# Kernel optimization log

Hardware: AMD Instinct MI355X
Metric: run time of the kernel (lower is better)

Reference implementation:

```python
import jax, jax.numpy as jnp
import numpy as np

# Module hyperparameters (from init_kwargs)
THRESHOLD_BASE = 1.0
TAU_MEM, TAU_SYN, TAU_ADAPT = 0.02, 0.005, 0.1
ADAPT_STRENGTH, HOMEO_RATE, DT = 0.1, 0.01, 0.001


def setup_inputs() -> dict:
    key = jax.random.key(0)
    B, F, T = 32, 8192, 128
    input_current = jax.random.normal(key, (B, F, T), dtype=jnp.float32)
    threshold_scale = jnp.ones((1,), dtype=jnp.float32)   # nn.Parameter(torch.ones(1))
    adaptation_bias = jnp.zeros((1,), dtype=jnp.float32)  # nn.Parameter(torch.zeros(1))
    return {"input_current": input_current,
            "threshold_scale": threshold_scale,
            "adaptation_bias": adaptation_bias}


def reference(input_current, threshold_scale, adaptation_bias):
    """Adaptive-threshold LIF neuron recurrence (AdaptiveThresholdLIFNeuron.forward).

    input_current: [B, F, T]
    Returns (spikes [B,F,T], membrane_trace [T], threshold_trace [T],
             final_firing_rate (scalar EMA), adaptation_state (scalar mean)).
    """
    B, F, T = input_current.shape
    dt = jnp.float32(DT)
    alpha = jnp.exp(-dt / TAU_MEM)   # membrane decay
    beta = jnp.exp(-dt / TAU_SYN)    # synaptic decay
    gamma = jnp.exp(-dt / TAU_ADAPT) # adaptation decay

    I_t = jnp.moveaxis(input_current, -1, 0)  # [T, B, F] for scan over time

    def step(carry, inp):
        membrane, synaptic, adaptation, ema = carry
        synaptic = beta * synaptic + inp
        membrane = alpha * membrane + synaptic
        # homeostatic component uses the running firing-rate EMA (scalar buffer)
        homeo = ADAPT_STRENGTH * jnp.maximum(ema - HOMEO_RATE, 0.0)
        adaptation = gamma * adaptation + (1.0 - gamma) * jax.lax.stop_gradient(membrane)
        threshold = (THRESHOLD_BASE * threshold_scale + homeo
                     + adaptation_bias + 0.1 * adaptation)  # [B, F]
        spike = (membrane >= threshold).astype(membrane.dtype)
        ema = 0.99 * ema + 0.01 * spike.mean()
        membrane = membrane - threshold * spike  # soft reset
        return (membrane, synaptic, adaptation, ema), (spike, membrane.mean(), threshold.mean())

    z = jnp.zeros((B, F), dtype=input_current.dtype)
    init = (z, z, z, jnp.zeros((), dtype=input_current.dtype))
    (membrane, synaptic, adaptation, ema), (spikes_t, mem_trace, thr_trace) = jax.lax.scan(step, init, I_t)

    spikes = jnp.moveaxis(spikes_t, 0, -1)  # [B, F, T]
    return spikes, mem_trace, thr_trace, ema, adaptation.mean()
```

## Files before the change

kernel.cpp:

```cpp
#include <hip/hip_runtime.h>
#include <math.h>

#pragma clang fp contract(off)

typedef unsigned int u32;

#define N_NEUR 262144
#define TT     128
#define OB     ((size_t)N_NEUR * TT)
#define PB     128
#define PT     512
#define NW     8
#define NREP   16
#define WGUARD (1 << 17)

__device__ __forceinline__ float wredf(float v) {
#pragma unroll
  for (int o = 32; o; o >>= 1) v += __shfl_xor(v, o);
  return v;
}
__device__ __forceinline__ int wredi(int v) {
#pragma unroll
  for (int o = 32; o; o >>= 1) v += __shfl_xor(v, o);
  return v;
}

__launch_bounds__(PT)
__global__ void snn_persist(const float* __restrict__ in, const float* __restrict__ tsp,
                            const float* __restrict__ abp, float* __restrict__ out,
                            u32* __restrict__ bits2, u32* __restrict__ g_rep,
                            float* __restrict__ wm, float* __restrict__ wt,
                            float* __restrict__ wa)
{
#pragma clang fp contract(off)
  const int tid  = threadIdx.x;
  const int bid  = blockIdx.x;
  const int gtid = bid * PT + tid;
  const int lane = tid & 63;
  const int wv   = tid >> 6;
  const int rep  = bid & (NREP - 1);

  const float alp = __uint_as_float(0x3F7383C5u);
  const float bet = __uint_as_float(0x3F519856u);
  const float gma = __uint_as_float(0x3F7D73E8u);
  const float omg = 1.0f - gma;
  const float tsv = tsp[0];
  const float abv = abp[0];

  const int n0 = gtid * 4;
  const float4* q0 = (const float4*)(in + (size_t)(n0 + 0) * TT);
  const float4* q1 = (const float4*)(in + (size_t)(n0 + 1) * TT);
  const float4* q2 = (const float4*)(in + (size_t)(n0 + 2) * TT);
  const float4* q3 = (const float4*)(in + (size_t)(n0 + 3) * TT);

  float4 c0 = q0[0], c1 = q1[0], c2 = q2[0], c3 = q3[0];
  float4 f0 = q0[1], f1 = q1[1], f2 = q2[1], f3 = q3[1];

  float S0,S1,S2,S3, Mp0,Mp1,Mp2,Mp3, A0,A1,A2,A3;
  S0 = __builtin_fmaf(bet, 0.0f, c0.x); Mp0 = __builtin_fmaf(alp, 0.0f, S0);
  A0 = __builtin_fmaf(gma, 0.0f, omg * Mp0);
  S1 = __builtin_fmaf(bet, 0.0f, c1.x); Mp1 = __builtin_fmaf(alp, 0.0f, S1);
  A1 = __builtin_fmaf(gma, 0.0f, omg * Mp1);
  S2 = __builtin_fmaf(bet, 0.0f, c2.x); Mp2 = __builtin_fmaf(alp, 0.0f, S2);
  A2 = __builtin_fmaf(gma, 0.0f, omg * Mp2);
  S3 = __builtin_fmaf(bet, 0.0f, c3.x); Mp3 = __builtin_fmaf(alp, 0.0f, S3);
  A3 = __builtin_fmaf(gma, 0.0f, omg * Mp3);

  float ema = 0.0f;
  float sc  = (tsv + 0.1f * fmaxf(0.0f - 0.01f, 0.0f)) + abv;

  __shared__ int   shc[NW];
  __shared__ float shm[NW];
  __shared__ u32   s_tot;

  float M0, M1, M2, M3;

#define STEP(T_, IN0, IN1, IN2, IN3) {                                         \
    const float th0 = __builtin_fmaf(0.1f, A0, sc);                            \
    const float th1 = __builtin_fmaf(0.1f, A1, sc);                            \
    const float th2 = __builtin_fmaf(0.1f, A2, sc);                            \
    const float th3 = __builtin_fmaf(0.1f, A3, sc);                            \
    const bool sp0 = (Mp0 >= th0);  M0 = sp0 ? Mp0 - th0 : Mp0;                \
    const bool sp1 = (Mp1 >= th1);  M1 = sp1 ? Mp1 - th1 : Mp1;                \
    const bool sp2 = (Mp2 >= th2);  M2 = sp2 ? Mp2 - th2 : Mp2;                \
    const bool sp3 = (Mp3 >= th3);  M3 = sp3 ? Mp3 - th3 : Mp3;                \
    int cnt = (int)sp0 + (int)sp1 + (int)sp2 + (int)sp3;                       \
    cnt = wredi(cnt);                                                          \
    if (lane == 0) shc[wv] = cnt;                                              \
    __syncthreads();                                                           \
    if (tid < NREP) {   \
      const int bc = ((((((shc[0] + shc[1]) + shc[2]) + shc[3]) + shc[4])      \
                       + shc[5]) + shc[6]) + shc[7];                           \
      __hip_atomic_store(&g_rep[((size_t)(T_) * NREP + tid) * PB + bid],       \
                         (u32)bc + 1u,                                         \
                         __ATOMIC_RELAXED, __HIP_MEMORY_SCOPE_AGENT);          \
    }                                                                          \
                        \
    u32 nib = (u32)sp0 | ((u32)sp1 << 1) | ((u32)sp2 << 2) | ((u32)sp3 << 3);  \
    u32 word = nib << (4 * (tid & 7));                                         \
    word |= (u32)__shfl_xor((int)word, 1);                                     \
    word |= (u32)__shfl_xor((int)word, 2);                                     \
    word |= (u32)__shfl_xor((int)word, 4);                                     \
    if ((tid & 7) == 0) bits2[(size_t)(gtid >> 3) * TT + (T_)] = word;         \
    float msum = ((M0 + M1) + M2) + M3;                                        \
    float tsum = ((th0 + th1) + th2) + th3;                                    \
    msum = wredf(msum); tsum = wredf(tsum);                                    \
    if (lane == 0) {                                                           \
      wm[((size_t)(T_) * PB + bid) * NW + wv] = msum;                          \
      wt[((size_t)(T_) * PB + bid) * NW + wv] = tsum;                          \
    }                                                                          \
    if ((T_) < TT - 1) {             \
      S0 = __builtin_fmaf(bet, S0, (IN0));                                     \
      Mp0 = __builtin_fmaf(alp, M0, S0);                                       \
      A0 = __builtin_fmaf(gma, A0, omg * Mp0);                                 \
      S1 = __builtin_fmaf(bet, S1, (IN1));                                     \
      Mp1 = __builtin_fmaf(alp, M1, S1);                                       \
      A1 = __builtin_fmaf(gma, A1, omg * Mp1);                                 \
      S2 = __builtin_fmaf(bet, S2, (IN2));                                     \
      Mp2 = __builtin_fmaf(alp, M2, S2);                                       \
      A2 = __builtin_fmaf(gma, A2, omg * Mp2);                                 \
      S3 = __builtin_fmaf(bet, S3, (IN3));                                     \
      Mp3 = __builtin_fmaf(alp, M3, S3);                                       \
      A3 = __builtin_fmaf(gma, A3, omg * Mp3);                                 \
    }                                                                          \
                        \
    if (wv == 0) {                                                             \
      const u32* slots_ = g_rep + ((size_t)(T_) * NREP + rep) * PB;            \
      u32 v0_, v1_; int gd_ = 0;                                               \
      while (1) {                                                              \
        v0_ = __hip_atomic_load(&slots_[lane],      __ATOMIC_RELAXED,          \
                                __HIP_MEMORY_SCOPE_AGENT);                     \
        v1_ = __hip_atomic_load(&slots_[lane + 64], __ATOMIC_RELAXED,          \
                                __HIP_MEMORY_SCOPE_AGENT);                     \
        if (__all(v0_ != 0u && v1_ != 0u)) break;                              \
        if (++gd_ > WGUARD) break;                                             \
      }                                                                        \
      int ss_ = (int)(v0_ ? v0_ - 1u : 0u) + (int)(v1_ ? v1_ - 1u : 0u);       \
      ss_ = wredi(ss_);                                                        \
      if (lane == 0) s_tot = (u32)ss_;                                         \
    }                                                                          \
    __syncthreads();                                                           \
    const float mean_ = (float)s_tot * 3.814697265625e-06f;        \
    ema = __builtin_fmaf(0.99f, ema, 0.01f * mean_);                           \
    sc  = (tsv + 0.1f * fmaxf(ema - 0.01f, 0.0f)) + abv;                       \
  }

#pragma unroll 1
  for (int q = 0; q < 32; ++q) {
    float4 p0 = {0,0,0,0}, p1 = {0,0,0,0}, p2 = {0,0,0,0}, p3 = {0,0,0,0};
    if (q < 30) { p0 = q0[q + 2]; p1 = q1[q + 2]; p2 = q2[q + 2]; p3 = q3[q + 2]; }
    const int tb = 4 * q;
    STEP(tb + 0, c0.y, c1.y, c2.y, c3.y)
    STEP(tb + 1, c0.z, c1.z, c2.z, c3.z)
    STEP(tb + 2, c0.w, c1.w, c2.w, c3.w)
    STEP(tb + 3, f0.x, f1.x, f2.x, f3.x)
    c0 = f0; c1 = f1; c2 = f2; c3 = f3;
    f0 = p0; f1 = p1; f2 = p2; f3 = p3;
  }
#undef STEP

  float asum = ((A0 + A1) + A2) + A3;
  asum = wredf(asum);
  if (lane == 0) shm[wv] = asum;
  __syncthreads();
  if (tid == 0) {
    float bs = 0.f;
    for (int w = 0; w < NW; ++w) bs += shm[w];
    wa[bid] = bs;
    if (bid == 0) out[OB + 256] = ema;
  }
}

__launch_bounds__(256)
__global__ void snn_finish(const float* __restrict__ wm, const float* __restrict__ wt,
                           const float* __restrict__ wa, float* __restrict__ out)
{
#pragma clang fp contract(off)
  const int tid = threadIdx.x;
  const float inv = 3.814697265625e-06f;
  if (tid < 128) {
    float s = 0.f;
    for (int j = 0; j < PB * NW; ++j) s += wm[(size_t)tid * PB * NW + j];
    out[OB + tid] = s * inv;
  } else {
    const int t = tid - 128;
    float s = 0.f;
    for (int j = 0; j < PB * NW; ++j) s += wt[(size_t)t * PB * NW + j];
    out[OB + 128 + t] = s * inv;
  }
  if (tid == 0) {
    float s = 0.f;
    for (int b = 0; b < PB; ++b) s += wa[b];
    out[OB + 257] = s * inv;
  }
}

__global__ void snn_expand(const u32* __restrict__ bits2, float* __restrict__ outF)
{
  const int gtid = blockIdx.x * blockDim.x + threadIdx.x;
  const int wave = gtid >> 6, lane = gtid & 63;
  const int nwaves = (gridDim.x * blockDim.x) >> 6;
  const int nloc = lane >> 5;
  const int tq   = lane & 31;
  for (int pair = wave; pair < N_NEUR / 2; pair += nwaves) {
    const int n = 2 * pair + nloc;
    const uint4 w = *(const uint4*)(bits2 + (size_t)(n >> 5) * TT + 4 * tq);
    const int b = n & 31;
    float4 f;
    f.x = (float)((w.x >> b) & 1u);
    f.y = (float)((w.y >> b) & 1u);
    f.z = (float)((w.z >> b) & 1u);
    f.w = (float)((w.w >> b) & 1u);
    ((float4*)outF)[(size_t)n * (TT / 4) + tq] = f;
  }
}

extern "C" void kernel_launch(void* const* d_in, const int* in_sizes, int n_in,
                              void* d_out, int out_size, void* d_ws, size_t ws_size,
                              hipStream_t stream)
{
  const float* in  = (const float*)d_in[0];
  const float* tsp = (const float*)d_in[1];
  const float* abp = (const float*)d_in[2];
  float* out = (float*)d_out;
  unsigned char* ws = (unsigned char*)d_ws;

  if (ws_size < 6292000u) return;

  u32*   bits2 = (u32*)(ws);
  float* wm    = (float*)(ws + 4194304);
  float* wt    = (float*)(ws + 4718592);
  u32*   g_rep = (u32*)(ws + 5242880);
  float* wa    = (float*)(ws + 6291456);

  hipMemsetAsync(g_rep, 0, 1048576, stream);

  snn_persist<<<dim3(PB), dim3(PT), 0, stream>>>(in, tsp, abp, out,
                                                 bits2, g_rep, wm, wt, wa);
  snn_finish<<<dim3(1), dim3(256), 0, stream>>>(wm, wt, wa, out);
  snn_expand<<<dim3(2048), dim3(256), 0, stream>>>(bits2, out);
}
```

Before: 370.4 us.

## Use 8 neurons per thread, 16-bit barrier slots, and backoff polling

Each thread now handles 8 neurons instead of 4, so blocks shrink to 256 threads and 4 waves. This is meant to make the per-timestep __syncthreads and intra-block reductions cheaper. Grid-barrier counters are packed as u16, so one 32-bit load per lane covers all 128 block slots during polling. Polling adds s_sleep backoff after 64 spins, and the spin guard drops from 131072 to 4096 iterations. That lower guard raises the risk of breaking early and using incomplete counts, while twice the registers per thread could hurt the latency hiding on the strided input loads.

```diff
diff --git a/kernel.cpp b/kernel.cpp
--- a/kernel.cpp
+++ b/kernel.cpp
@@ -4,15 +4,17 @@
 #pragma clang fp contract(off)
 
 typedef unsigned int u32;
+typedef unsigned short u16;
 
 #define N_NEUR 262144
 #define TT     128
 #define OB     ((size_t)N_NEUR * TT)
 #define PB     128
-#define PT     512
-#define NW     8
+#define PT     256
+#define NW     4
+#define NN     8
 #define NREP   16
-#define WGUARD (1 << 17)
+#define WGUARD 4096
 
 __device__ __forceinline__ float wredf(float v) {
 #pragma unroll
@@ -28,7 +30,7 @@
 __launch_bounds__(PT)
 __global__ void snn_persist(const float* __restrict__ in, const float* __restrict__ tsp,
                             const float* __restrict__ abp, float* __restrict__ out,
-                            u32* __restrict__ bits2, u32* __restrict__ g_rep,
+                            u32* __restrict__ bits2, u16* __restrict__ g_rep,
                             float* __restrict__ wm, float* __restrict__ wt,
                             float* __restrict__ wa)
 {
@@ -47,24 +49,23 @@
   const float tsv = tsp[0];
   const float abv = abp[0];
 
-  const int n0 = gtid * 4;
-  const float4* q0 = (const float4*)(in + (size_t)(n0 + 0) * TT);
-  const float4* q1 = (const float4*)(in + (size_t)(n0 + 1) * TT);
-  const float4* q2 = (const float4*)(in + (size_t)(n0 + 2) * TT);
-  const float4* q3 = (const float4*)(in + (size_t)(n0 + 3) * TT);
-
-  float4 c0 = q0[0], c1 = q1[0], c2 = q2[0], c3 = q3[0];
-  float4 f0 = q0[1], f1 = q1[1], f2 = q2[1], f3 = q3[1];
-
-  float S0,S1,S2,S3, Mp0,Mp1,Mp2,Mp3, A0,A1,A2,A3;
-  S0 = __builtin_fmaf(bet, 0.0f, c0.x); Mp0 = __builtin_fmaf(alp, 0.0f, S0);
-  A0 = __builtin_fmaf(gma, 0.0f, omg * Mp0);
-  S1 = __builtin_fmaf(bet, 0.0f, c1.x); Mp1 = __builtin_fmaf(alp, 0.0f, S1);
-  A1 = __builtin_fmaf(gma, 0.0f, omg * Mp1);
-  S2 = __builtin_fmaf(bet, 0.0f, c2.x); Mp2 = __builtin_fmaf(alp, 0.0f, S2);
-  A2 = __builtin_fmaf(gma, 0.0f, omg * Mp2);
-  S3 = __builtin_fmaf(bet, 0.0f, c3.x); Mp3 = __builtin_fmaf(alp, 0.0f, S3);
-  A3 = __builtin_fmaf(gma, 0.0f, omg * Mp3);
+  const int n0 = gtid * NN;
+  const float4* q[NN];
+#pragma unroll
+  for (int j = 0; j < NN; ++j)
+    q[j] = (const float4*)(in + (size_t)(n0 + j) * TT);
+
+  float4 c[NN], f[NN];
+#pragma unroll
+  for (int j = 0; j < NN; ++j) { c[j] = q[j][0]; f[j] = q[j][1]; }
+
+  float S[NN], Mp[NN], A[NN], M[NN];
+#pragma unroll
+  for (int j = 0; j < NN; ++j) {
+    S[j]  = __builtin_fmaf(bet, 0.0f, c[j].x);
+    Mp[j] = __builtin_fmaf(alp, 0.0f, S[j]);
+    A[j]  = __builtin_fmaf(gma, 0.0f, omg * Mp[j]);
+  }
 
   float ema = 0.0f;
   float sc  = (tsv + 0.1f * fmaxf(0.0f - 0.01f, 0.0f)) + abv;
@@ -73,69 +74,66 @@
   __shared__ float shm[NW];
   __shared__ u32   s_tot;
 
-  float M0, M1, M2, M3;
-
-#define STEP(T_, IN0, IN1, IN2, IN3) {                                         \
-    const float th0 = __builtin_fmaf(0.1f, A0, sc);                            \
-    const float th1 = __builtin_fmaf(0.1f, A1, sc);                            \
-    const float th2 = __builtin_fmaf(0.1f, A2, sc);                            \
-    const float th3 = __builtin_fmaf(0.1f, A3, sc);                            \
-    const bool sp0 = (Mp0 >= th0);  M0 = sp0 ? Mp0 - th0 : Mp0;                \
-    const bool sp1 = (Mp1 >= th1);  M1 = sp1 ? Mp1 - th1 : Mp1;                \
-    const bool sp2 = (Mp2 >= th2);  M2 = sp2 ? Mp2 - th2 : Mp2;                \
-    const bool sp3 = (Mp3 >= th3);  M3 = sp3 ? Mp3 - th3 : Mp3;                \
-    int cnt = (int)sp0 + (int)sp1 + (int)sp2 + (int)sp3;                       \
+  const u32* g32 = (const u32*)g_rep;
+
+#define STEP(T_, INEXPR) {                                                     \
+    u32 nib = 0; int cnt = 0;                                                  \
+    _Pragma("unroll")                                                          \
+    for (int j = 0; j < NN; ++j) {                                             \
+      const float th_ = __builtin_fmaf(0.1f, A[j], sc);                        \
+      const bool sp_ = (Mp[j] >= th_);                                         \
+      M[j] = sp_ ? Mp[j] - th_ : Mp[j];                                        \
+      cnt += (int)sp_;                                                         \
+      nib |= ((u32)sp_) << j;                                                  \
+    }                                                                          \
     cnt = wredi(cnt);                                                          \
     if (lane == 0) shc[wv] = cnt;                                              \
     __syncthreads();                                                           \
-    if (tid < NREP) {   \
-      const int bc = ((((((shc[0] + shc[1]) + shc[2]) + shc[3]) + shc[4])      \
-                       + shc[5]) + shc[6]) + shc[7];                           \
+    if (tid < NREP) {                                                          \
+      const int bc = ((shc[0] + shc[1]) + shc[2]) + shc[3];                    \
       __hip_atomic_store(&g_rep[((size_t)(T_) * NREP + tid) * PB + bid],       \
-                         (u32)bc + 1u,                                         \
+                         (u16)(bc + 1),                                        \
                          __ATOMIC_RELAXED, __HIP_MEMORY_SCOPE_AGENT);          \
     }                                                                          \
+    asm volatile("" ::: "memory");   \
                         \
-    u32 nib = (u32)sp0 | ((u32)sp1 << 1) | ((u32)sp2 << 2) | ((u32)sp3 << 3);  \
-    u32 word = nib << (4 * (tid & 7));                                         \
+    u32 word = nib << (8 * (tid & 3));                                         \
     word |= (u32)__shfl_xor((int)word, 1);                                     \
     word |= (u32)__shfl_xor((int)word, 2);                                     \
-    word |= (u32)__shfl_xor((int)word, 4);                                     \
-    if ((tid & 7) == 0) bits2[(size_t)(gtid >> 3) * TT + (T_)] = word;         \
-    float msum = ((M0 + M1) + M2) + M3;                                        \
-    float tsum = ((th0 + th1) + th2) + th3;                                    \
+    if ((tid & 3) == 0) bits2[(size_t)(gtid >> 2) * TT + (T_)] = word;         \
+    float msum = 0.f, tsum = 0.f;                                              \
+    _Pragma("unroll")                                                          \
+    for (int j = 0; j < NN; ++j) {                                             \
+      msum += M[j];                                                            \
+      tsum += __builtin_fmaf(0.1f, A[j], sc);      \
+    }                                                                          \
     msum = wredf(msum); tsum = wredf(tsum);                                    \
     if (lane == 0) {                                                           \
       wm[((size_t)(T_) * PB + bid) * NW + wv] = msum;                          \
       wt[((size_t)(T_) * PB + bid) * NW + wv] = tsum;                          \
     }                                                                          \
-    if ((T_) < TT - 1) {             \
-      S0 = __builtin_fmaf(bet, S0, (IN0));                                     \
-      Mp0 = __builtin_fmaf(alp, M0, S0);                                       \
-      A0 = __builtin_fmaf(gma, A0, omg * Mp0);                                 \
-      S1 = __builtin_fmaf(bet, S1, (IN1));                                     \
-      Mp1 = __builtin_fmaf(alp, M1, S1);                                       \
-      A1 = __builtin_fmaf(gma, A1, omg * Mp1);                                 \
-      S2 = __builtin_fmaf(bet, S2, (IN2));                                     \
-      Mp2 = __builtin_fmaf(alp, M2, S2);                                       \
-      A2 = __builtin_fmaf(gma, A2, omg * Mp2);                                 \
-      S3 = __builtin_fmaf(bet, S3, (IN3));                                     \
-      Mp3 = __builtin_fmaf(alp, M3, S3);                                       \
-      A3 = __builtin_fmaf(gma, A3, omg * Mp3);                                 \
-    }                                                                          \
-                        \
+    if ((T_) < TT - 1) {                  \
+      _Pragma("unroll")                                                        \
+      for (int j = 0; j < NN; ++j) {                                           \
+        const float I_ = (INEXPR);                                             \
+        S[j]  = __builtin_fmaf(bet, S[j], I_);                                 \
+        Mp[j] = __builtin_fmaf(alp, M[j], S[j]);                               \
+        A[j]  = __builtin_fmaf(gma, A[j], omg * Mp[j]);                        \
+      }                                                                        \
+    }                                                                          \
+                     \
     if (wv == 0) {                                                             \
-      const u32* slots_ = g_rep + ((size_t)(T_) * NREP + rep) * PB;            \
-      u32 v0_, v1_; int gd_ = 0;                                               \
+      const u32* pollp = g32 + ((size_t)(T_) * NREP + rep) * (PB / 2);         \
+      u32 v_; int gd_ = 0;                                                     \
       while (1) {                                                              \
-        v0_ = __hip_atomic_load(&slots_[lane],      __ATOMIC_RELAXED,          \
-                                __HIP_MEMORY_SCOPE_AGENT);                     \
-        v1_ = __hip_atomic_load(&slots_[lane + 64], __ATOMIC_RELAXED,          \
-                                __HIP_MEMORY_SCOPE_AGENT);                     \
-        if (__all(v0_ != 0u && v1_ != 0u)) break;                              \
+        v_ = __hip_atomic_load(&pollp[lane], __ATOMIC_RELAXED,                 \
+                               __HIP_MEMORY_SCOPE_AGENT);                      \
+        if (__all(((v_ & 0xFFFFu) != 0u) && ((v_ >> 16) != 0u))) break;        \
         if (++gd_ > WGUARD) break;                                             \
+        if (gd_ > 64) __builtin_amdgcn_s_sleep(1);                             \
       }                                                                        \
-      int ss_ = (int)(v0_ ? v0_ - 1u : 0u) + (int)(v1_ ? v1_ - 1u : 0u);       \
+      const u32 lo_ = v_ & 0xFFFFu, hi_ = v_ >> 16;                            \
+      int ss_ = (int)(lo_ ? lo_ - 1u : 0u) + (int)(hi_ ? hi_ - 1u : 0u);       \
       ss_ = wredi(ss_);                                                        \
       if (lane == 0) s_tot = (u32)ss_;                                         \
     }                                                                          \
@@ -146,26 +144,32 @@
   }
 
 #pragma unroll 1
-  for (int q = 0; q < 32; ++q) {
-    float4 p0 = {0,0,0,0}, p1 = {0,0,0,0}, p2 = {0,0,0,0}, p3 = {0,0,0,0};
-    if (q < 30) { p0 = q0[q + 2]; p1 = q1[q + 2]; p2 = q2[q + 2]; p3 = q3[q + 2]; }
-    const int tb = 4 * q;
-    STEP(tb + 0, c0.y, c1.y, c2.y, c3.y)
-    STEP(tb + 1, c0.z, c1.z, c2.z, c3.z)
-    STEP(tb + 2, c0.w, c1.w, c2.w, c3.w)
-    STEP(tb + 3, f0.x, f1.x, f2.x, f3.x)
-    c0 = f0; c1 = f1; c2 = f2; c3 = f3;
-    f0 = p0; f1 = p1; f2 = p2; f3 = p3;
+  for (int qq = 0; qq < 32; ++qq) {
+    float4 p[NN];
+#pragma unroll
+    for (int j = 0; j < NN; ++j) p[j] = make_float4(0.f, 0.f, 0.f, 0.f);
+    if (qq < 30) {
+#pragma unroll
+      for (int j = 0; j < NN; ++j) p[j] = q[j][qq + 2];
+    }
+    const int tb = 4 * qq;
+    STEP(tb + 0, c[j].y)
+    STEP(tb + 1, c[j].z)
+    STEP(tb + 2, c[j].w)
+    STEP(tb + 3, f[j].x)
+#pragma unroll
+    for (int j = 0; j < NN; ++j) { c[j] = f[j]; f[j] = p[j]; }
   }
 #undef STEP
 
-  float asum = ((A0 + A1) + A2) + A3;
+  float asum = 0.f;
+#pragma unroll
+  for (int j = 0; j < NN; ++j) asum += A[j];
   asum = wredf(asum);
   if (lane == 0) shm[wv] = asum;
   __syncthreads();
   if (tid == 0) {
-    float bs = 0.f;
-    for (int w = 0; w < NW; ++w) bs += shm[w];
+    float bs = ((shm[0] + shm[1]) + shm[2]) + shm[3];
     wa[bid] = bs;
     if (bid == 0) out[OB + 256] = ema;
   }
@@ -225,15 +229,15 @@
   float* out = (float*)d_out;
   unsigned char* ws = (unsigned char*)d_ws;
 
-  if (ws_size < 6292000u) return;
-
-  u32*   bits2 = (u32*)(ws);
-  float* wm    = (float*)(ws + 4194304);
-  float* wt    = (float*)(ws + 4718592);
-  u32*   g_rep = (u32*)(ws + 5242880);
-  float* wa    = (float*)(ws + 6291456);
-
-  hipMemsetAsync(g_rep, 0, 1048576, stream);
+  if (ws_size < 5243392u) return;
+
+  u32* bits2 = (u32*)(ws);
+  u16* g_rep = (u16*)(ws + 4194304);
+  float* wm  = (float*)(ws + 4718592);
+  float* wt  = (float*)(ws + 4980736);
+  float* wa  = (float*)(ws + 5242880);
+
+  hipMemsetAsync(g_rep, 0, 524288, stream);
 
   snn_persist<<<dim3(PB), dim3(PT), 0, stream>>>(in, tsp, abp, out,
                                                  bits2, g_rep, wm, wt, wa);
```

Result: slower. 447.6 us (+20.8%).
